# Performance work log

Hardware: AMD Instinct MI355X
Metric: run time of the kernel (lower is better)

Reference implementation:

```python
import jax, jax.numpy as jnp
import numpy as np

N_GRAPHS = 64
NEG_SLOPE = 0.01  # default LeakyReLU slope
BN_EPS = 1e-5


def setup_inputs() -> dict:
    key = jax.random.key(0)
    ks = jax.random.split(key, 16)
    N, E, F_IN, H, H2, OUT, L = 50000, 800000, 64, 128, 64, 8, 3
    return {
        "x": jax.random.normal(ks[0], (N, F_IN), jnp.float32),
        "edge_index": jax.random.randint(ks[1], (2, E), 0, N, jnp.int32),
        "batch": jnp.sort(jax.random.randint(ks[2], (N,), 0, N_GRAPHS, jnp.int32)),
        "W_emb": jax.random.normal(ks[3], (F_IN, H), jnp.float32) * 0.05,
        "b_emb": jnp.zeros((H,), jnp.float32),
        "convW": jax.random.normal(ks[4], (L, H, H), jnp.float32) * 0.05,
        "convB": jnp.zeros((L, H), jnp.float32),
        "bn_gamma": jax.random.uniform(ks[5], (L, H), jnp.float32) + 0.5,
        "bn_beta": jax.random.normal(ks[6], (L, H), jnp.float32) * 0.1,
        "bn_mean": jax.random.normal(ks[7], (L, H), jnp.float32) * 0.1,
        "bn_var": jax.random.uniform(ks[8], (L, H), jnp.float32) + 0.5,
        "W1": jax.random.normal(ks[9], (H, H2), jnp.float32) * 0.05,
        "b1": jnp.zeros((H2,), jnp.float32),
        "W2": jax.random.normal(ks[10], (H2, OUT), jnp.float32) * 0.05,
        "b2": jnp.zeros((OUT,), jnp.float32),
    }


def reference(x, edge_index, batch, W_emb, b_emb, convW, convB,
              bn_gamma, bn_beta, bn_mean, bn_var, W1, b1, W2, b2):
    N = x.shape[0]
    # GCN normalization with self-loops (computed once; identical per layer)
    loop = jnp.arange(N, dtype=edge_index.dtype)
    s = jnp.concatenate([edge_index[0], loop])  # [E+N]
    d = jnp.concatenate([edge_index[1], loop])
    deg = jax.ops.segment_sum(jnp.ones(d.shape, x.dtype), d, num_segments=N)
    dinv = jax.lax.rsqrt(deg)  # deg >= 1 thanks to self-loops
    norm = dinv[s] * dinv[d]  # [E+N]

    h = x @ W_emb + b_emb  # node embedding, [N, H]
    L = convW.shape[0]
    for i in range(L):
        m = h @ convW[i]  # linear transform, [N, H]
        # gather-weight-scatter: sum_{(s->d)} norm * m[s]
        agg = jax.ops.segment_sum(m[s] * norm[:, None], d, num_segments=N) + convB[i]
        # BatchNorm (eval mode, running stats)
        hbn = (agg - bn_mean[i]) * jax.lax.rsqrt(bn_var[i] + BN_EPS) * bn_gamma[i] + bn_beta[i]
        h = jnp.where(hbn > 0, hbn, NEG_SLOPE * hbn)  # LeakyReLU
        # dropout is identity in eval mode

    g = jax.ops.segment_sum(h, batch, num_segments=N_GRAPHS)  # global_add_pool, [G, H]
    z = g @ W1 + b1
    z = jnp.where(z > 0, z, NEG_SLOPE * z)
    return z @ W2 + b2  # [G, OUT]
```

## Files before the change

### kernel.cpp

```cpp
#include <hip/hip_runtime.h>

#define NEG 0.01f
#define HF 128
#define BK 64
#define PB 512
#define SEG 40

typedef __attribute__((ext_vector_type(8))) short bf8;
typedef __attribute__((ext_vector_type(4))) float f4;
typedef __attribute__((ext_vector_type(2))) float f2;

__device__ __forceinline__ unsigned short f2bf(float v) {
    unsigned u = __float_as_uint(v);
    u = (u + 0x7fff + ((u >> 16) & 1)) >> 16;
    return (unsigned short)u;
}

__global__ __launch_bounds__(256) void k_mega1(
        const int* __restrict__ src, const int* __restrict__ dst, int E,
        int* __restrict__ cellcnt, int2* __restrict__ binbuf,
        const float* __restrict__ x, const float* __restrict__ W_emb,
        const float* __restrict__ b_emb, short* __restrict__ hbuf, int N,
        const float* __restrict__ convW, short* __restrict__ wt_c, int L,
        const float* __restrict__ convB,
        const float* __restrict__ bn_g, const float* __restrict__ bn_b,
        const float* __restrict__ bn_m, const float* __restrict__ bn_v,
        float* __restrict__ scb, float* __restrict__ shb,
        int NBIN, int EB, int WB) {
    __shared__ short wt[128 * 88];
    __shared__ int lcur[256];
    const int bid = blockIdx.x;
    const int tid = threadIdx.x;

    if (bid < PB) {
        lcur[tid] = 0;
        __syncthreads();
        const int per = (E + PB - 1) / PB;
        const int e0 = bid * per;
        const int e1 = (e0 + per < E) ? e0 + per : E;
        for (int e = e0 + tid; e < e1; e += 256) {
            const int d = dst[e];
            const int b = d >> 8;
            const int p = atomicAdd(&lcur[b], 1);
            if (p < SEG)
                binbuf[((size_t)b * PB + bid) * SEG + p] = make_int2(src[e], d);
        }
        __syncthreads();
        if (tid < NBIN) {
            int c = lcur[tid];
            cellcnt[(size_t)tid * PB + bid] = c < SEG ? c : SEG;
        }
        return;
    }
    if (bid < PB + EB) {
        for (int i = tid; i < 128 * 64; i += 256) {
            const int n = i >> 6, k = i & 63;
            wt[n * 88 + k] = (short)f2bf(W_emb[(size_t)k * HF + n]);
        }
        __syncthreads();
        const int wid = tid >> 6, lane = tid & 63;
        const int lr = lane & 15, lk = lane >> 4;
        const int m0 = (bid - PB) * 64 + wid * 16;
        if (m0 >= N) return;
        const int arow_i = m0 + lr < N ? m0 + lr : N - 1;
        bf8 a[2];
        const float* arow = x + (size_t)arow_i * 64 + lk * 8;
#pragma unroll
        for (int kk = 0; kk < 2; ++kk) {
            const float4 p = *reinterpret_cast<const float4*>(arow + kk * 32);
            const float4 q = *reinterpret_cast<const float4*>(arow + kk * 32 + 4);
            bf8 t;
            t[0] = (short)f2bf(p.x); t[1] = (short)f2bf(p.y);
            t[2] = (short)f2bf(p.z); t[3] = (short)f2bf(p.w);
            t[4] = (short)f2bf(q.x); t[5] = (short)f2bf(q.y);
            t[6] = (short)f2bf(q.z); t[7] = (short)f2bf(q.w);
            a[kk] = t;
        }
#pragma unroll
        for (int n = 0; n < 8; ++n) {
            f4 acc = {0.f, 0.f, 0.f, 0.f};
            const short* brow = wt + (n * 16 + lr) * 88 + lk * 8;
#pragma unroll
            for (int kk = 0; kk < 2; ++kk) {
                const bf8 b = *reinterpret_cast<const bf8*>(brow + kk * 32);
                acc = __builtin_amdgcn_mfma_f32_16x16x32_bf16(a[kk], b, acc, 0, 0, 0);
            }
            const int col = n * 16 + lr;
            const float bs = b_emb[col];
#pragma unroll
            for (int r = 0; r < 4; ++r)
                hbuf[(size_t)(m0 + lk * 4 + r) * HF + col] = (short)f2bf(acc[r] + bs);
        }
        return;
    }
    if (bid < PB + EB + WB) {
        const int i = (bid - PB - EB) * 256 + tid;
        const int per = HF * HF;
        if (i < L * per) {
            const int l = i / per, r = i % per;
            const int n = r / HF, k = r % HF;
            wt_c[i] = (short)f2bf(convW[(size_t)l * per + (size_t)k * HF + n]);
        }
        return;
    }
    const int i = (bid - PB - EB - WB) * 256 + tid;
    if (i < L * HF) {
        const float s = rsqrtf(bn_v[i] + 1e-5f) * bn_g[i];
        scb[i] = s;
        shb[i] = (convB[i] - bn_m[i]) * s + bn_b[i];
    }
}

__global__ __launch_bounds__(256) void k_binfill(
        const int* __restrict__ cellcnt, const int2* __restrict__ binbuf,
        int* __restrict__ bkt, int* __restrict__ cnt,
        float* __restrict__ gbuf, short* __restrict__ mzero,
        int NBIN, int ZROFF) {
    const int bid = blockIdx.x;
    const int tid = threadIdx.x;
    if (bid >= NBIN) {
        for (int i = tid; i < 64 * HF; i += 256) gbuf[i] = 0.0f;
        if (tid < 64) reinterpret_cast<int*>(mzero)[tid] = 0;
        return;
    }
    __shared__ int lcnt[256];
    lcnt[tid] = 0;
    __syncthreads();
    for (int sg = tid; sg < PB; sg += 256) {
        const int c = cellcnt[(size_t)bid * PB + sg];
        const int2* segp = binbuf + ((size_t)bid * PB + sg) * SEG;
        for (int i = 0; i < c; ++i) {
            const int2 ed = segp[i];
            const int p = atomicAdd(&lcnt[ed.y & 255], 1);
            if (p < BK) bkt[(size_t)ed.y * BK + p] = ed.x << 8;
        }
    }
    __syncthreads();
    int c = lcnt[tid];
    if (c > BK) c = BK;
    const int pc = (c + 7) & ~7;
    const int node = (bid << 8) + tid;
    for (int p = c; p < pc; ++p) bkt[(size_t)node * BK + p] = ZROFF;
    cnt[node] = c;
}

__global__ __launch_bounds__(256) void k_gemm_conv(
        const short* __restrict__ A,
        const short* __restrict__ Bt,
        const int* __restrict__ cnt,
        short* __restrict__ C,
        int N) {
    const int tid = threadIdx.x;
    const int wid = tid >> 6, lane = tid & 63;
    const int lr = lane & 15, lk = lane >> 4;
    const int m0 = blockIdx.x * 128 + wid * 32;
    if (m0 >= N) return;
    bf8 aA[4], aB[4];
    const short* arowA = A + (size_t)(m0 + lr) * HF + lk * 8;
    const short* arowB = arowA + 16 * HF;
#pragma unroll
    for (int kk = 0; kk < 4; ++kk) {
        aA[kk] = *reinterpret_cast<const bf8*>(arowA + kk * 32);
        aB[kk] = *reinterpret_cast<const bf8*>(arowB + kk * 32);
    }
    float dvA[4], dvB[4];
#pragma unroll
    for (int r = 0; r < 4; ++r) {
        int rowA = m0 + lk * 4 + r;       if (rowA >= N) rowA = N - 1;
        int rowB = m0 + 16 + lk * 4 + r;  if (rowB >= N) rowB = N - 1;
        dvA[r] = rsqrtf((float)cnt[rowA] + 1.0f);
        dvB[r] = rsqrtf((float)cnt[rowB] + 1.0f);
    }
#pragma unroll
    for (int n = 0; n < 8; ++n) {
        f4 accA = {0.f, 0.f, 0.f, 0.f};
        f4 accB = {0.f, 0.f, 0.f, 0.f};
        const short* brow = Bt + (size_t)(n * 16 + lr) * HF + lk * 8;
#pragma unroll
        for (int kk = 0; kk < 4; ++kk) {
            const bf8 b = *reinterpret_cast<const bf8*>(brow + kk * 32);
            accA = __builtin_amdgcn_mfma_f32_16x16x32_bf16(aA[kk], b, accA, 0, 0, 0);
            accB = __builtin_amdgcn_mfma_f32_16x16x32_bf16(aB[kk], b, accB, 0, 0, 0);
        }
        const int col = n * 16 + lr;
#pragma unroll
        for (int r = 0; r < 4; ++r) {
            C[(size_t)(m0 + lk * 4 + r) * HF + col]      = (short)f2bf(accA[r] * dvA[r]);
            C[(size_t)(m0 + 16 + lk * 4 + r) * HF + col] = (short)f2bf(accB[r] * dvB[r]);
        }
    }
}

__global__ __launch_bounds__(256) void k_gather(
        const int* __restrict__ bkt, const int* __restrict__ cnt,
        const short* __restrict__ ms,
        const float* __restrict__ sc, const float* __restrict__ sh,
        short* __restrict__ h, int N) {
    const int wid  = (blockIdx.x * 256 + threadIdx.x) >> 6;
    const int lane = threadIdx.x & 63;
    const int sub  = lane >> 4;
    const int lf   = lane & 15;
    if (wid >= N) return;
    const size_t b0 = (size_t)wid * BK;
    const int myoff = bkt[b0 + lane];
    const int deg = cnt[wid];
    const int pdeg = (deg + 7) & ~7;

    f2 acc[4];
#pragma unroll
    for (int j = 0; j < 4; ++j) acc[j] = (f2){0.f, 0.f};
    union U { bf8 v; unsigned u[4]; };

    U self;
    self.v = *reinterpret_cast<const bf8*>(ms + (size_t)wid * HF + lf * 8);

    const char* msb = (const char*)ms + lf * 16;
    for (int t = sub; t < pdeg; t += 8) {
        const int o0 = __shfl(myoff, t);
        const int o1 = __shfl(myoff, t + 4);
        U a, b;
        a.v = *reinterpret_cast<const bf8*>(msb + o0);
        b.v = *reinterpret_cast<const bf8*>(msb + o1);
#pragma unroll
        for (int j = 0; j < 4; ++j) {
            f2 va, vb;
            va.x = __uint_as_float(a.u[j] << 16);
            va.y = __uint_as_float(a.u[j] & 0xffff0000u);
            vb.x = __uint_as_float(b.u[j] << 16);
            vb.y = __uint_as_float(b.u[j] & 0xffff0000u);
            acc[j] += va + vb;
        }
    }
    if (sub == 0) {
#pragma unroll
        for (int j = 0; j < 4; ++j) {
            f2 val;
            val.x = __uint_as_float(self.u[j] << 16);
            val.y = __uint_as_float(self.u[j] & 0xffff0000u);
            acc[j] += val;
        }
    }
#pragma unroll
    for (int j = 0; j < 4; ++j) {
        acc[j].x += __shfl_xor(acc[j].x, 16);
        acc[j].y += __shfl_xor(acc[j].y, 16);
        acc[j].x += __shfl_xor(acc[j].x, 32);
        acc[j].y += __shfl_xor(acc[j].y, 32);
    }
    if (sub == 0) {
        const float dv = rsqrtf((float)deg + 1.0f);
        const int f0 = lf * 8;
        const float4 sca = *reinterpret_cast<const float4*>(sc + f0);
        const float4 scb2 = *reinterpret_cast<const float4*>(sc + f0 + 4);
        const float4 sha = *reinterpret_cast<const float4*>(sh + f0);
        const float4 shb2 = *reinterpret_cast<const float4*>(sh + f0 + 4);
        const float scv[8] = {sca.x, sca.y, sca.z, sca.w, scb2.x, scb2.y, scb2.z, scb2.w};
        const float shv[8] = {sha.x, sha.y, sha.z, sha.w, shb2.x, shb2.y, shb2.z, shb2.w};
        unsigned ou[4];
#pragma unroll
        for (int j = 0; j < 4; ++j) {
            float vx = fmaf(acc[j].x * dv, scv[2 * j],     shv[2 * j]);
            float vy = fmaf(acc[j].y * dv, scv[2 * j + 1], shv[2 * j + 1]);
            vx = fmaxf(vx, NEG * vx);
            vy = fmaxf(vy, NEG * vy);
            ou[j] = (unsigned)f2bf(vx) | ((unsigned)f2bf(vy) << 16);
        }
        *reinterpret_cast<uint4*>(h + (size_t)wid * HF + f0) =
            *reinterpret_cast<uint4*>(ou);
    }
}

__global__ __launch_bounds__(256) void k_pool(
        const short* __restrict__ h, const int* __restrict__ batch,
        float* __restrict__ g, int N, int per) {
    const int gwid = (blockIdx.x * 256 + threadIdx.x) >> 6;
    const int lane = threadIdx.x & 63;
    const int n0 = gwid * per;
    if (n0 >= N) return;
    const int n1 = (n0 + per < N) ? n0 + per : N;
    const int fp = lane * 2;
    float ax = 0.f, ay = 0.f;
    int cur = batch[n0];
    for (int n = n0; n < n1; ++n) {
        const int b = batch[n];
        if (b != cur) {
            atomicAdd(&g[cur * HF + fp], ax);
            atomicAdd(&g[cur * HF + fp + 1], ay);
            ax = 0.f; ay = 0.f; cur = b;
        }
        const unsigned u = *reinterpret_cast<const unsigned*>(h + (size_t)n * HF + fp);
        ax += __uint_as_float(u << 16);
        ay += __uint_as_float(u & 0xffff0000u);
    }
    atomicAdd(&g[cur * HF + fp], ax);
    atomicAdd(&g[cur * HF + fp + 1], ay);
}

__global__ __launch_bounds__(128) void k_mlp(
        const float* __restrict__ g, const float* __restrict__ W1,
        const float* __restrict__ b1, const float* __restrict__ W2,
        const float* __restrict__ b2, float* __restrict__ out) {
    __shared__ float gr[128];
    __shared__ float z[64];
    const int gid = blockIdx.x, t = threadIdx.x;
    gr[t] = g[gid * HF + t];
    __syncthreads();
    if (t < 64) {
        float acc = b1[t];
#pragma unroll 8
        for (int k = 0; k < 128; ++k) acc += gr[k] * W1[k * 64 + t];
        z[t] = acc > 0.0f ? acc : NEG * acc;
    }
    __syncthreads();
    if (t < 8) {
        float acc = b2[t];
#pragma unroll 8
        for (int j = 0; j < 64; ++j) acc += z[j] * W2[j * 8 + t];
        out[gid * 8 + t] = acc;
    }
}

extern "C" void kernel_launch(void* const* d_in, const int* in_sizes, int n_in,
                              void* d_out, int out_size, void* d_ws, size_t ws_size,
                              hipStream_t stream) {
    const float* x       = (const float*)d_in[0];
    const int*   eidx    = (const int*)  d_in[1];
    const int*   batch   = (const int*)  d_in[2];
    const float* W_emb   = (const float*)d_in[3];
    const float* b_emb   = (const float*)d_in[4];
    const float* convW   = (const float*)d_in[5];
    const float* convB   = (const float*)d_in[6];
    const float* bn_g    = (const float*)d_in[7];
    const float* bn_b    = (const float*)d_in[8];
    const float* bn_m    = (const float*)d_in[9];
    const float* bn_v    = (const float*)d_in[10];
    const float* W1      = (const float*)d_in[11];
    const float* b1      = (const float*)d_in[12];
    const float* W2      = (const float*)d_in[13];
    const float* b2      = (const float*)d_in[14];

    const int F_IN = 64;
    const int N = in_sizes[0] / F_IN;
    const int E = in_sizes[1] / 2;
    const int L = in_sizes[5] / (HF * HF);
    const int G = 64;

    const int* esrc = eidx;
    const int* edst = eidx + E;

    const int NBIN  = (N + 255) >> 8;
    const int Npad2 = NBIN << 8;
    const int Npad  = ((N + 127) / 128) * 128;

    int* bkt      = (int*)d_ws;
    int* cnt      = bkt + (size_t)Npad2 * BK;
    int* cellcnt  = cnt + Npad2;
    int2* binbuf  = (int2*)(cellcnt + (size_t)NBIN * PB);
    short* hbuf   = (short*)(binbuf + (size_t)NBIN * PB * SEG);
    short* ms     = hbuf + (size_t)Npad * HF;
    short* wt_c   = ms + (size_t)(Npad + 128) * HF;
    float* gbuf   = (float*)(wt_c + (size_t)L * HF * HF);
    float* scb    = gbuf + G * HF;
    float* shb    = scb + L * HF;

    const int ZROFF = Npad * HF * 2;

    const int EB = (N + 63) / 64;
    const int WB = (L * HF * HF + 255) / 256;
    const int SB = (L * HF + 255) / 256;
    k_mega1<<<PB + EB + WB + SB, 256, 0, stream>>>(
        esrc, edst, E, cellcnt, binbuf, x, W_emb, b_emb, hbuf, N,
        convW, wt_c, L, convB, bn_g, bn_b, bn_m, bn_v, scb, shb,
        NBIN, EB, WB);

    k_binfill<<<NBIN + 1, 256, 0, stream>>>(
        cellcnt, binbuf, bkt, cnt, gbuf, ms + (size_t)Npad * HF, NBIN, ZROFF);

    for (int i = 0; i < L; ++i) {
        k_gemm_conv<<<(N + 127) / 128, 256, 0, stream>>>(
            hbuf, wt_c + (size_t)i * HF * HF, cnt, ms, N);
        k_gather<<<(N * 64 + 255) / 256, 256, 0, stream>>>(
            bkt, cnt, ms, scb + i * HF, shb + i * HF, hbuf, N);
    }

    const int nwaves = 256 * 4;
    const int per = (N + nwaves - 1) / nwaves;
    k_pool<<<256, 256, 0, stream>>>(hbuf, batch, gbuf, N, per);
    k_mlp<<<G, 128, 0, stream>>>(gbuf, W1, b1, W2, b2, (float*)d_out);
}
```

Before: 212.4 us.

## Pack binned edges into one int and sort per-node neighbor lists in LDS

Each binned edge is now stored as a single packed int (source offset shifted left 8 bits, OR'd with the local destination), which halves binbuf traffic. In binfill, the first LSL neighbors of each node are collected in shared memory and insertion-sorted by source offset before being written to the bucket. Sorted neighbor lists should make the later gather over source rows more cache-local. In exchange, binfill uses about 41KB of extra LDS per block and does a serial per-thread sort, and packing the source id into 24 bits limits how many nodes are supported.

```diff
diff --git a/kernel.cpp b/kernel.cpp
--- a/kernel.cpp
+++ b/kernel.cpp
@@ -5,6 +5,7 @@
 #define BK 64
 #define PB 512
 #define SEG 40
+#define LSL 40
 
 typedef __attribute__((ext_vector_type(8))) short bf8;
 typedef __attribute__((ext_vector_type(4))) float f4;
@@ -18,7 +19,7 @@
 
 __global__ __launch_bounds__(256) void k_mega1(
         const int* __restrict__ src, const int* __restrict__ dst, int E,
-        int* __restrict__ cellcnt, int2* __restrict__ binbuf,
+        int* __restrict__ cellcnt, int* __restrict__ binbuf,
         const float* __restrict__ x, const float* __restrict__ W_emb,
         const float* __restrict__ b_emb, short* __restrict__ hbuf, int N,
         const float* __restrict__ convW, short* __restrict__ wt_c, int L,
@@ -43,7 +44,7 @@
             const int b = d >> 8;
             const int p = atomicAdd(&lcur[b], 1);
             if (p < SEG)
-                binbuf[((size_t)b * PB + bid) * SEG + p] = make_int2(src[e], d);
+                binbuf[((size_t)b * PB + bid) * SEG + p] = (src[e] << 8) | (d & 255);
         }
         __syncthreads();
         if (tid < NBIN) {
@@ -112,7 +113,7 @@
 }
 
 __global__ __launch_bounds__(256) void k_binfill(
-        const int* __restrict__ cellcnt, const int2* __restrict__ binbuf,
+        const int* __restrict__ cellcnt, const int* __restrict__ binbuf,
         int* __restrict__ bkt, int* __restrict__ cnt,
         float* __restrict__ gbuf, short* __restrict__ mzero,
         int NBIN, int ZROFF) {
@@ -124,23 +125,37 @@
         return;
     }
     __shared__ int lcnt[256];
+    __shared__ int sbuf[256][LSL + 1];
     lcnt[tid] = 0;
     __syncthreads();
     for (int sg = tid; sg < PB; sg += 256) {
         const int c = cellcnt[(size_t)bid * PB + sg];
-        const int2* segp = binbuf + ((size_t)bid * PB + sg) * SEG;
+        const int* segp = binbuf + ((size_t)bid * PB + sg) * SEG;
         for (int i = 0; i < c; ++i) {
-            const int2 ed = segp[i];
-            const int p = atomicAdd(&lcnt[ed.y & 255], 1);
-            if (p < BK) bkt[(size_t)ed.y * BK + p] = ed.x << 8;
+            const int ed = segp[i];
+            const int dl = ed & 255;
+            const int off = ed & ~255;
+            const int p = atomicAdd(&lcnt[dl], 1);
+            if (p < LSL) sbuf[dl][p] = off;
+            else if (p < BK)
+                bkt[(size_t)((bid << 8) + dl) * BK + p] = off;
         }
     }
     __syncthreads();
     int c = lcnt[tid];
     if (c > BK) c = BK;
+    const int m = c < LSL ? c : LSL;
+    for (int i = 1; i < m; ++i) {
+        const int key = sbuf[tid][i];
+        int j = i - 1;
+        while (j >= 0 && sbuf[tid][j] > key) { sbuf[tid][j + 1] = sbuf[tid][j]; --j; }
+        sbuf[tid][j + 1] = key;
+    }
+    const int node = (bid << 8) + tid;
+    int* brow = bkt + (size_t)node * BK;
+    for (int p = 0; p < m; ++p) brow[p] = sbuf[tid][p];
     const int pc = (c + 7) & ~7;
-    const int node = (bid << 8) + tid;
-    for (int p = c; p < pc; ++p) bkt[(size_t)node * BK + p] = ZROFF;
+    for (int p = c; p < pc; ++p) brow[p] = ZROFF;
     cnt[node] = c;
 }
 
@@ -355,7 +370,7 @@
     int* bkt      = (int*)d_ws;
     int* cnt      = bkt + (size_t)Npad2 * BK;
     int* cellcnt  = cnt + Npad2;
-    int2* binbuf  = (int2*)(cellcnt + (size_t)NBIN * PB);
+    int* binbuf   = cellcnt + (size_t)NBIN * PB;
     short* hbuf   = (short*)(binbuf + (size_t)NBIN * PB * SEG);
     short* ms     = hbuf + (size_t)Npad * HF;
     short* wt_c   = ms + (size_t)(Npad + 128) * HF;
```

Measured after the change: 250.1 us. +17.7%, slower.
